# Kernel optimization log

Hardware: AMD Instinct MI355X
Metric: run time of the kernel (lower is better)

## Reference

```python
import jax, jax.numpy as jnp
import numpy as np

N_NODES = 100000


def setup_inputs() -> dict:
    key = jax.random.key(0)
    k1, k2, k3, k4, k5 = jax.random.split(key, 5)
    n_edges = 1600000
    d_in, d_out = 128, 128
    input_features = jax.random.normal(k1, (N_NODES, d_in), dtype=jnp.float32)
    weight = jax.random.normal(k2, (d_in, d_out), dtype=jnp.float32) * (1.0 / np.sqrt(d_out))
    edge_vals = jax.random.uniform(k3, (n_edges,), dtype=jnp.float32)
    edge_src = jax.random.randint(k4, (n_edges,), 0, N_NODES, dtype=jnp.int32)
    edge_dst = jax.random.randint(k5, (n_edges,), 0, N_NODES, dtype=jnp.int32)
    return {
        "input_features": input_features,
        "weight": weight,
        "edge_vals": edge_vals,
        "edge_src": edge_src,
        "edge_dst": edge_dst,
    }


def reference(input_features, weight, edge_vals, edge_src, edge_dst):
    neg_slope = 0.0
    # dense transform: support = X @ W  -> [N, d_out]
    support = input_features @ weight
    # sparse SpMM: out[dst] += val * support[src]  (COO adjacency)
    msgs = edge_vals[:, None] * support[edge_src]  # [E, d_out]
    output = jax.ops.segment_sum(msgs, edge_dst, num_segments=N_NODES)
    # leaky_relu with negative_slope = neg_slope (0 -> relu)
    return jnp.where(output >= 0, output, neg_slope * output)
```

## Files before the change

### kernel.cpp

```cpp
#include <hip/hip_runtime.h>
#include <hip/hip_bf16.h>


#define D 128
#define NB_SHIFT 6
#define BNODES 64
#define MAXB 2048
#define CAPB 1408
#define RPT 6
#define XSTR 136
#define NFILL 256
#define GROWS 128

using bf16x8 = __attribute__((ext_vector_type(8))) short;
using f32x4  = __attribute__((ext_vector_type(4))) float;

__device__ inline unsigned short f2bf(float f) {
    unsigned u = __float_as_uint(f);
    u += 0x7fffu + ((u >> 16) & 1u);
    return (unsigned short)(u >> 16);
}
__device__ inline float bflo(unsigned w) { return __uint_as_float(w << 16); }
__device__ inline float bfhi(unsigned w) { return __uint_as_float(w & 0xffff0000u); }

__global__ __launch_bounds__(256) void wtrans(const float* __restrict__ W,
                                              unsigned short* __restrict__ WT,
                                              int* cursor, int nb) {
    const int t = threadIdx.x, b = blockIdx.x;
    const int n  = (b << 4) | (t & 15);
    const int k0 = (t >> 4) << 3;
#pragma unroll
    for (int k = k0; k < k0 + 8; ++k)
        WT[n * D + k] = f2bf(W[k * D + n]);
    if (b == 0)
        for (int i = t; i < nb; i += 256) cursor[i] = 0;
}

#define SMEM_BYTES (GROWS * XSTR * 2 + 128 * XSTR * 2)

__device__ void gemm_path(const float* __restrict__ X,
                          const unsigned short* __restrict__ WT,
                          unsigned short* __restrict__ S,
                          int nRows, int blk, char* smem) {
    unsigned short* Xl = (unsigned short*)smem;
    unsigned short* Wl = (unsigned short*)(smem + GROWS * XSTR * 2);

    const int t = threadIdx.x;
    const int row0 = blk * GROWS;

    const uint4* WT4 = (const uint4*)WT;
    uint4* Wl4 = (uint4*)Wl;
#pragma unroll
    for (int i = t; i < 2048; i += 1024) {
        int n = i >> 4, kc8 = i & 15;
        Wl4[n * (XSTR / 8) + kc8] = WT4[i];
    }

    const float4* X4 = (const float4*)X;
    ushort4* Xl4 = (ushort4*)Xl;
#pragma unroll
    for (int i = t; i < 4096; i += 1024) {
        int r = i >> 5, c = i & 31;
        int gr = row0 + r;
        float4 v = make_float4(0.f, 0.f, 0.f, 0.f);
        if (gr < nRows) v = X4[(size_t)gr * 32 + c];
        ushort4 p;
        p.x = f2bf(v.x); p.y = f2bf(v.y); p.z = f2bf(v.z); p.w = f2bf(v.w);
        Xl4[r * (XSTR / 4) + c] = p;
    }
    __syncthreads();

    const int wv = t >> 6, lane = t & 63;
    const int m = lane & 15, quad = lane >> 4;
    const int m0  = (wv & 7) << 4;
    const int nt0 = (wv >> 3) << 2;

    f32x4 acc[4];
    f32x4 z = {0.f, 0.f, 0.f, 0.f};
#pragma unroll
    for (int nt = 0; nt < 4; ++nt) acc[nt] = z;

#pragma unroll
    for (int kc = 0; kc < 4; ++kc) {
        bf16x8 a = *(const bf16x8*)(Xl + (m0 + m) * XSTR + kc * 32 + quad * 8);
#pragma unroll
        for (int nt = 0; nt < 4; ++nt) {
            bf16x8 b = *(const bf16x8*)(Wl + ((nt0 + nt) * 16 + m) * XSTR + kc * 32 + quad * 8);
            acc[nt] = __builtin_amdgcn_mfma_f32_16x16x32_bf16(a, b, acc[nt], 0, 0, 0);
        }
    }

#pragma unroll
    for (int nt = 0; nt < 4; ++nt) {
#pragma unroll
        for (int r = 0; r < 4; ++r) {
            int gr = row0 + m0 + quad * 4 + r;
            if (gr < nRows)
                S[(size_t)gr * D + (nt0 + nt) * 16 + m] = f2bf(acc[nt][r]);
        }
    }
}

__device__ void fill2_path(const int* __restrict__ src,
                           const int* __restrict__ dst,
                           const float* __restrict__ vals,
                           int* gcursor, int2* __restrict__ epk,
                           int E, int nb, int blk, char* smem) {
    int* h   = (int*)smem;
    int* cur = (int*)(smem + MAXB * 4);
    const int t = threadIdx.x;
    for (int i = t; i < nb; i += 1024) h[i] = 0;
    __syncthreads();

    int chunk = (E + NFILL - 1) / NFILL;
    chunk = (chunk + 3) & ~3;
    const int s0 = min(E, blk * chunk);
    const int s1 = min(E, s0 + chunk);
    const int vend = s0 + ((s1 - s0) & ~3);

    const int e0 = s0 + (t << 2);
    const int e1 = e0 + 4096;
    int4 rs0, rd0, rs1, rd1;
    float4 rv0, rv1;
    const bool has0 = (e0 + 4 <= vend);
    const bool has1 = (e1 + 4 <= vend);
    if (has0) {
        rd0 = *(const int4*)(dst + e0);
        rs0 = *(const int4*)(src + e0);
        rv0 = *(const float4*)(vals + e0);
        atomicAdd(&h[rd0.x >> NB_SHIFT], 1);
        atomicAdd(&h[rd0.y >> NB_SHIFT], 1);
        atomicAdd(&h[rd0.z >> NB_SHIFT], 1);
        atomicAdd(&h[rd0.w >> NB_SHIFT], 1);
    }
    if (has1) {
        rd1 = *(const int4*)(dst + e1);
        rs1 = *(const int4*)(src + e1);
        rv1 = *(const float4*)(vals + e1);
        atomicAdd(&h[rd1.x >> NB_SHIFT], 1);
        atomicAdd(&h[rd1.y >> NB_SHIFT], 1);
        atomicAdd(&h[rd1.z >> NB_SHIFT], 1);
        atomicAdd(&h[rd1.w >> NB_SHIFT], 1);
    }
    for (int e = vend + t; e < s1; e += 1024)
        atomicAdd(&h[dst[e] >> NB_SHIFT], 1);
    __syncthreads();

    for (int i = t; i < nb; i += 1024) {
        int c = h[i];
        cur[i] = c ? (i * CAPB + atomicAdd(&gcursor[i], c)) : 0;
    }
    __syncthreads();

    if (has0) {
        int p0 = atomicAdd(&cur[rd0.x >> NB_SHIFT], 1);
        int p1 = atomicAdd(&cur[rd0.y >> NB_SHIFT], 1);
        int p2 = atomicAdd(&cur[rd0.z >> NB_SHIFT], 1);
        int p3 = atomicAdd(&cur[rd0.w >> NB_SHIFT], 1);
        epk[p0] = make_int2(rs0.x | ((rd0.x & (BNODES - 1)) << 20), __float_as_int(rv0.x));
        epk[p1] = make_int2(rs0.y | ((rd0.y & (BNODES - 1)) << 20), __float_as_int(rv0.y));
        epk[p2] = make_int2(rs0.z | ((rd0.z & (BNODES - 1)) << 20), __float_as_int(rv0.z));
        epk[p3] = make_int2(rs0.w | ((rd0.w & (BNODES - 1)) << 20), __float_as_int(rv0.w));
    }
    if (has1) {
        int p0 = atomicAdd(&cur[rd1.x >> NB_SHIFT], 1);
        int p1 = atomicAdd(&cur[rd1.y >> NB_SHIFT], 1);
        int p2 = atomicAdd(&cur[rd1.z >> NB_SHIFT], 1);
        int p3 = atomicAdd(&cur[rd1.w >> NB_SHIFT], 1);
        epk[p0] = make_int2(rs1.x | ((rd1.x & (BNODES - 1)) << 20), __float_as_int(rv1.x));
        epk[p1] = make_int2(rs1.y | ((rd1.y & (BNODES - 1)) << 20), __float_as_int(rv1.y));
        epk[p2] = make_int2(rs1.z | ((rd1.z & (BNODES - 1)) << 20), __float_as_int(rv1.z));
        epk[p3] = make_int2(rs1.w | ((rd1.w & (BNODES - 1)) << 20), __float_as_int(rv1.w));
    }
    for (int e = vend + t; e < s1; e += 1024) {
        int d = dst[e];
        int pos = atomicAdd(&cur[d >> NB_SHIFT], 1);
        epk[pos] = make_int2(src[e] | ((d & (BNODES - 1)) << 20), __float_as_int(vals[e]));
    }
}

__global__ __launch_bounds__(1024, 8) void fused_pre(const float* __restrict__ X,
                                                     const unsigned short* __restrict__ WT,
                                                     unsigned short* __restrict__ S,
                                                     int nRows,
                                                     const int* __restrict__ src,
                                                     const int* __restrict__ dst,
                                                     const float* __restrict__ vals,
                                                     int* gcursor, int2* __restrict__ epk,
                                                     int E, int nb) {
    __shared__ char smem[SMEM_BYTES];
    const int bid = blockIdx.x;
    if (bid < NFILL)
        fill2_path(src, dst, vals, gcursor, epk, E, nb, bid, smem);
    else
        gemm_path(X, WT, S, nRows, bid - NFILL, smem);
}

#define ACC8(e, mm) { float v = __int_as_float(e.y);                         \
    a[0] = fmaf(v, bflo(mm.x), a[0]); a[1] = fmaf(v, bfhi(mm.x), a[1]);      \
    a[2] = fmaf(v, bflo(mm.y), a[2]); a[3] = fmaf(v, bfhi(mm.y), a[3]);      \
    a[4] = fmaf(v, bflo(mm.z), a[4]); a[5] = fmaf(v, bfhi(mm.z), a[5]);      \
    a[6] = fmaf(v, bflo(mm.w), a[6]); a[7] = fmaf(v, bfhi(mm.w), a[7]); }

__global__ __launch_bounds__(256, 8) void bucket_gather(const unsigned short* __restrict__ support,
                                                        const int* __restrict__ gcursor,
                                                        const int2* __restrict__ epk,
                                                        float* __restrict__ out, int N) {
    __shared__ int2 se[CAPB];
    __shared__ int  hist[BNODES];
    __shared__ int  rows[BNODES];
    __shared__ int  cur[BNODES];

    const int t    = threadIdx.x;
    const int b    = blockIdx.x >> 1;
    const int half = blockIdx.x & 1;
    const int cnt  = min(gcursor[b], CAPB);
    const int beg  = b * CAPB;

    if (t < BNODES) hist[t] = 0;
    __syncthreads();

    int2 r[RPT];
#pragma unroll
    for (int i = 0; i < RPT; ++i) {
        int idx = t + (i << 8);
        if (idx < cnt) r[i] = epk[beg + idx];
    }
#pragma unroll
    for (int i = 0; i < RPT; ++i) {
        int idx = t + (i << 8);
        if (idx < cnt) atomicAdd(&hist[(r[i].x >> 20) & (BNODES - 1)], 1);
    }
    __syncthreads();

    if (t < BNODES) rows[t] = hist[t];
    __syncthreads();
#pragma unroll
    for (int off = 1; off < BNODES; off <<= 1) {
        int v = 0;
        if (t < BNODES && t >= off) v = rows[t - off];
        __syncthreads();
        if (t < BNODES && t >= off) rows[t] += v;
        __syncthreads();
    }
    if (t < BNODES) cur[t] = rows[t] - hist[t];
    __syncthreads();

#pragma unroll
    for (int i = 0; i < RPT; ++i) {
        int idx = t + (i << 8);
        if (idx < cnt) {
            int pos = atomicAdd(&cur[(r[i].x >> 20) & (BNODES - 1)], 1);
            se[pos] = r[i];
        }
    }
    __syncthreads();

    const int g = t >> 3, lane = t & 7;
    const int node0 = b << NB_SHIFT;
    const int colbase = half << 3;
    const uint4* S4 = (const uint4*)support;
    float4* o4 = (float4*)out;

#pragma unroll
    for (int nn = g; nn < BNODES; nn += 32) {
        const int send = rows[nn];
        const int sbeg = send - hist[nn];

        float a[8];
#pragma unroll
        for (int k = 0; k < 8; ++k) a[k] = 0.f;

        int j = sbeg;
        for (; j + 4 <= send; j += 4) {
            int2 e0 = se[j], e1 = se[j + 1], e2 = se[j + 2], e3 = se[j + 3];
            uint4 m0 = S4[(size_t)(e0.x & 0xFFFFF) * 16 + colbase + lane];
            uint4 m1 = S4[(size_t)(e1.x & 0xFFFFF) * 16 + colbase + lane];
            uint4 m2 = S4[(size_t)(e2.x & 0xFFFFF) * 16 + colbase + lane];
            uint4 m3 = S4[(size_t)(e3.x & 0xFFFFF) * 16 + colbase + lane];
            ACC8(e0, m0); ACC8(e1, m1); ACC8(e2, m2); ACC8(e3, m3);
        }
        for (; j < send; ++j) {
            int2 e0 = se[j];
            uint4 m0 = S4[(size_t)(e0.x & 0xFFFFF) * 16 + colbase + lane];
            ACC8(e0, m0);
        }

        const int gn = node0 + nn;
        if (gn < N) {
            size_t base = (size_t)gn * 32 + (half << 4) + 2 * lane;
            float4 lo = make_float4(fmaxf(a[0], 0.f), fmaxf(a[1], 0.f),
                                    fmaxf(a[2], 0.f), fmaxf(a[3], 0.f));
            float4 hi = make_float4(fmaxf(a[4], 0.f), fmaxf(a[5], 0.f),
                                    fmaxf(a[6], 0.f), fmaxf(a[7], 0.f));
            o4[base]     = lo;
            o4[base + 1] = hi;
        }
    }
}

extern "C" void kernel_launch(void* const* d_in, const int* in_sizes, int n_in,
                              void* d_out, int out_size, void* d_ws, size_t ws_size,
                              hipStream_t stream) {
    const float* X    = (const float*)d_in[0];
    const float* W    = (const float*)d_in[1];
    const float* vals = (const float*)d_in[2];
    const int*   src  = (const int*)d_in[3];
    const int*   dst  = (const int*)d_in[4];
    float*       out  = (float*)d_out;

    const int N  = in_sizes[0] / D;
    const int E  = in_sizes[2];
    const int nb = (N + BNODES - 1) / BNODES;

    size_t off = 0;
    auto take = [&](size_t bytes) {
        size_t p = off;
        off = (off + bytes + 255) & ~(size_t)255;
        return p;
    };
    char* ws = (char*)d_ws;
    size_t o_support = take((size_t)N * D * sizeof(unsigned short));
    size_t o_wt      = take((size_t)D * D * sizeof(unsigned short));
    size_t o_cursor  = take((size_t)nb * sizeof(int));
    size_t o_epk     = take(((size_t)nb * CAPB + 1024) * sizeof(int2));
    (void)ws_size;

    unsigned short* support = (unsigned short*)(ws + o_support);
    unsigned short* WT      = (unsigned short*)(ws + o_wt);
    int*  cursor = (int*)(ws + o_cursor);
    int2* epk    = (int2*)(ws + o_epk);

    wtrans<<<8, 256, 0, stream>>>(W, WT, cursor, nb);

    const int nbG = (N + GROWS - 1) / GROWS;
    fused_pre<<<NFILL + nbG, 1024, 0, stream>>>(X, WT, support, N,
                                                src, dst, vals, cursor, epk, E, nb);

    bucket_gather<<<2 * nb, 256, 0, stream>>>(support, cursor, epk, out, N);
}
```

Measured before the change: 196.1 us.

## Quantize support matrix to per-row int8 and regroup gather block ordering

The GEMM epilogue now computes a per-row absolute max through shared-memory atomics. It quantizes the support matrix to offset uint8 with a per-row float scale instead of bf16, which halves the bytes fetched per edge in the random gather. The gather folds the scale into the edge weight, dequantizes by subtracting 128 times the sum of weighted scales, and remaps block indices so both column halves of 8 buckets sit close together in launch order. This trades accuracy (8-bit mantissa-like precision per row) for lower gather bandwidth, and adds one extra scale load per edge.

```diff
diff --git a/kernel.cpp b/kernel.cpp
--- a/kernel.cpp
+++ b/kernel.cpp
@@ -20,8 +20,6 @@
     u += 0x7fffu + ((u >> 16) & 1u);
     return (unsigned short)(u >> 16);
 }
-__device__ inline float bflo(unsigned w) { return __uint_as_float(w << 16); }
-__device__ inline float bfhi(unsigned w) { return __uint_as_float(w & 0xffff0000u); }
 
 __global__ __launch_bounds__(256) void wtrans(const float* __restrict__ W,
                                               unsigned short* __restrict__ WT,
@@ -36,17 +34,21 @@
         for (int i = t; i < nb; i += 256) cursor[i] = 0;
 }
 
-#define SMEM_BYTES (GROWS * XSTR * 2 + 128 * XSTR * 2)
+#define SMEM_BYTES (GROWS * XSTR * 2 + 128 * XSTR * 2 + GROWS * 4)
 
 __device__ void gemm_path(const float* __restrict__ X,
                           const unsigned short* __restrict__ WT,
-                          unsigned short* __restrict__ S,
+                          unsigned char* __restrict__ S8,
+                          float* __restrict__ scaleArr,
                           int nRows, int blk, char* smem) {
     unsigned short* Xl = (unsigned short*)smem;
     unsigned short* Wl = (unsigned short*)(smem + GROWS * XSTR * 2);
+    int* rowAmaxI = (int*)(smem + GROWS * XSTR * 2 + 128 * XSTR * 2);
 
     const int t = threadIdx.x;
     const int row0 = blk * GROWS;
+
+    if (t < GROWS) rowAmaxI[t] = 0;
 
     const uint4* WT4 = (const uint4*)WT;
     uint4* Wl4 = (uint4*)Wl;
@@ -91,12 +93,29 @@
     }
 
 #pragma unroll
-    for (int nt = 0; nt < 4; ++nt) {
-#pragma unroll
-        for (int r = 0; r < 4; ++r) {
-            int gr = row0 + m0 + quad * 4 + r;
-            if (gr < nRows)
-                S[(size_t)gr * D + (nt0 + nt) * 16 + m] = f2bf(acc[nt][r]);
+    for (int r = 0; r < 4; ++r) {
+        float lm = fabsf(acc[0][r]);
+        lm = fmaxf(lm, fabsf(acc[1][r]));
+        lm = fmaxf(lm, fabsf(acc[2][r]));
+        lm = fmaxf(lm, fabsf(acc[3][r]));
+        atomicMax(&rowAmaxI[m0 + quad * 4 + r], __float_as_int(lm));
+    }
+    __syncthreads();
+
+#pragma unroll
+    for (int r = 0; r < 4; ++r) {
+        const int row = m0 + quad * 4 + r;
+        const int gr = row0 + row;
+        const float rm = __int_as_float(rowAmaxI[row]);
+        const float inv = rm > 0.f ? 127.f / rm : 0.f;
+        if (gr < nRows) {
+#pragma unroll
+            for (int nt = 0; nt < 4; ++nt) {
+                int q = __float2int_rn(acc[nt][r] * inv) + 128;
+                S8[(size_t)gr * D + (nt0 + nt) * 16 + m] = (unsigned char)q;
+            }
+            if (m == 0 && nt0 == 0)
+                scaleArr[gr] = rm * (1.f / 127.f);
         }
     }
 }
@@ -181,7 +200,8 @@
 
 __global__ __launch_bounds__(1024, 8) void fused_pre(const float* __restrict__ X,
                                                      const unsigned short* __restrict__ WT,
-                                                     unsigned short* __restrict__ S,
+                                                     unsigned char* __restrict__ S8,
+                                                     float* __restrict__ scaleArr,
                                                      int nRows,
                                                      const int* __restrict__ src,
                                                      const int* __restrict__ dst,
@@ -193,27 +213,35 @@
     if (bid < NFILL)
         fill2_path(src, dst, vals, gcursor, epk, E, nb, bid, smem);
     else
-        gemm_path(X, WT, S, nRows, bid - NFILL, smem);
-}
-
-#define ACC8(e, mm) { float v = __int_as_float(e.y);                         \
-    a[0] = fmaf(v, bflo(mm.x), a[0]); a[1] = fmaf(v, bfhi(mm.x), a[1]);      \
-    a[2] = fmaf(v, bflo(mm.y), a[2]); a[3] = fmaf(v, bfhi(mm.y), a[3]);      \
-    a[4] = fmaf(v, bflo(mm.z), a[4]); a[5] = fmaf(v, bfhi(mm.z), a[5]);      \
-    a[6] = fmaf(v, bflo(mm.w), a[6]); a[7] = fmaf(v, bfhi(mm.w), a[7]); }
-
-__global__ __launch_bounds__(256, 8) void bucket_gather(const unsigned short* __restrict__ support,
+        gemm_path(X, WT, S8, scaleArr, nRows, bid - NFILL, smem);
+}
+
+#define ACCQ(vs, mm) {                                                        \
+    a[0] = fmaf(vs, (float)((mm.x) & 0xffu), a[0]);                           \
+    a[1] = fmaf(vs, (float)((mm.x >> 8) & 0xffu), a[1]);                      \
+    a[2] = fmaf(vs, (float)((mm.x >> 16) & 0xffu), a[2]);                     \
+    a[3] = fmaf(vs, (float)(mm.x >> 24), a[3]);                               \
+    a[4] = fmaf(vs, (float)((mm.y) & 0xffu), a[4]);                           \
+    a[5] = fmaf(vs, (float)((mm.y >> 8) & 0xffu), a[5]);                      \
+    a[6] = fmaf(vs, (float)((mm.y >> 16) & 0xffu), a[6]);                     \
+    a[7] = fmaf(vs, (float)(mm.y >> 24), a[7]); }
+
+__global__ __launch_bounds__(256, 8) void bucket_gather(const unsigned char* __restrict__ S8,
+                                                        const float* __restrict__ scaleArr,
                                                         const int* __restrict__ gcursor,
                                                         const int2* __restrict__ epk,
-                                                        float* __restrict__ out, int N) {
+                                                        float* __restrict__ out, int N, int nb) {
     __shared__ int2 se[CAPB];
     __shared__ int  hist[BNODES];
     __shared__ int  rows[BNODES];
     __shared__ int  cur[BNODES];
 
     const int t    = threadIdx.x;
-    const int b    = blockIdx.x >> 1;
-    const int half = blockIdx.x & 1;
+    const int grp  = blockIdx.x >> 4;
+    const int rem  = blockIdx.x & 15;
+    const int half = rem >> 3;
+    const int b    = (grp << 3) + (rem & 7);
+    if (b >= nb) return;
     const int cnt  = min(gcursor[b], CAPB);
     const int beg  = b * CAPB;
 
@@ -258,8 +286,7 @@
 
     const int g = t >> 3, lane = t & 7;
     const int node0 = b << NB_SHIFT;
-    const int colbase = half << 3;
-    const uint4* S4 = (const uint4*)support;
+    const int cb = (half << 6) + (lane << 3);
     float4* o4 = (float4*)out;
 
 #pragma unroll
@@ -270,21 +297,35 @@
         float a[8];
 #pragma unroll
         for (int k = 0; k < 8; ++k) a[k] = 0.f;
+        float svs = 0.f;
 
         int j = sbeg;
         for (; j + 4 <= send; j += 4) {
             int2 e0 = se[j], e1 = se[j + 1], e2 = se[j + 2], e3 = se[j + 3];
-            uint4 m0 = S4[(size_t)(e0.x & 0xFFFFF) * 16 + colbase + lane];
-            uint4 m1 = S4[(size_t)(e1.x & 0xFFFFF) * 16 + colbase + lane];
-            uint4 m2 = S4[(size_t)(e2.x & 0xFFFFF) * 16 + colbase + lane];
-            uint4 m3 = S4[(size_t)(e3.x & 0xFFFFF) * 16 + colbase + lane];
-            ACC8(e0, m0); ACC8(e1, m1); ACC8(e2, m2); ACC8(e3, m3);
+            const int s0i = e0.x & 0xFFFFF, s1i = e1.x & 0xFFFFF;
+            const int s2i = e2.x & 0xFFFFF, s3i = e3.x & 0xFFFFF;
+            uint2 m0 = *(const uint2*)(S8 + ((size_t)s0i << 7) + cb);
+            uint2 m1 = *(const uint2*)(S8 + ((size_t)s1i << 7) + cb);
+            uint2 m2 = *(const uint2*)(S8 + ((size_t)s2i << 7) + cb);
+            uint2 m3 = *(const uint2*)(S8 + ((size_t)s3i << 7) + cb);
+            float vs0 = __int_as_float(e0.y) * scaleArr[s0i];
+            float vs1 = __int_as_float(e1.y) * scaleArr[s1i];
+            float vs2 = __int_as_float(e2.y) * scaleArr[s2i];
+            float vs3 = __int_as_float(e3.y) * scaleArr[s3i];
+            svs += (vs0 + vs1) + (vs2 + vs3);
+            ACCQ(vs0, m0); ACCQ(vs1, m1); ACCQ(vs2, m2); ACCQ(vs3, m3);
         }
         for (; j < send; ++j) {
             int2 e0 = se[j];
-            uint4 m0 = S4[(size_t)(e0.x & 0xFFFFF) * 16 + colbase + lane];
-            ACC8(e0, m0);
-        }
+            const int s0i = e0.x & 0xFFFFF;
+            uint2 m0 = *(const uint2*)(S8 + ((size_t)s0i << 7) + cb);
+            float vs0 = __int_as_float(e0.y) * scaleArr[s0i];
+            svs += vs0;
+            ACCQ(vs0, m0);
+        }
+
+#pragma unroll
+        for (int k = 0; k < 8; ++k) a[k] = fmaf(-128.f, svs, a[k]);
 
         const int gn = node0 + nn;
         if (gn < N) {
@@ -320,22 +361,25 @@
         return p;
     };
     char* ws = (char*)d_ws;
-    size_t o_support = take((size_t)N * D * sizeof(unsigned short));
+    size_t o_support = take((size_t)N * D);
+    size_t o_scale   = take((size_t)N * sizeof(float));
     size_t o_wt      = take((size_t)D * D * sizeof(unsigned short));
     size_t o_cursor  = take((size_t)nb * sizeof(int));
     size_t o_epk     = take(((size_t)nb * CAPB + 1024) * sizeof(int2));
     (void)ws_size;
 
-    unsigned short* support = (unsigned short*)(ws + o_support);
-    unsigned short* WT      = (unsigned short*)(ws + o_wt);
+    unsigned char*  S8       = (unsigned char*)(ws + o_support);
+    float*          scaleArr = (float*)(ws + o_scale);
+    unsigned short* WT       = (unsigned short*)(ws + o_wt);
     int*  cursor = (int*)(ws + o_cursor);
     int2* epk    = (int2*)(ws + o_epk);
 
     wtrans<<<8, 256, 0, stream>>>(W, WT, cursor, nb);
 
     const int nbG = (N + GROWS - 1) / GROWS;
-    fused_pre<<<NFILL + nbG, 1024, 0, stream>>>(X, WT, support, N,
+    fused_pre<<<NFILL + nbG, 1024, 0, stream>>>(X, WT, S8, scaleArr, N,
                                                 src, dst, vals, cursor, epk, E, nb);
 
-    bucket_gather<<<2 * nb, 256, 0, stream>>>(support, cursor, epk, out, N);
-}
+    const int gblocks = ((nb + 7) / 8) * 16;
+    bucket_gather<<<gblocks, 256, 0, stream>>>(S8, scaleArr, cursor, epk, out, N, nb);
+}
```

Measured after the change: 192.2 us. 1.02x faster.
